# Kernel tuning notes

Measured on AMD Instinct MI355X. Metric: run time of the kernel, lower is better.

Reference implementation:

```python
import jax, jax.numpy as jnp
import numpy as np

BINS = 10
LOSS_WEIGHT = 1.0


def setup_inputs() -> dict:
    key = jax.random.key(0)
    k1, k2 = jax.random.split(key)
    B, C = 16384, 1000
    logits = jax.random.normal(k1, (B, C), dtype=jnp.float32)
    target_indices = jax.random.randint(k2, (B,), 0, C)
    return {"logits": logits, "target_indices": target_indices}


def reference(logits, target_indices):
    B, C = logits.shape
    bins = BINS
    target = jax.nn.one_hot(target_indices, C, dtype=logits.dtype)  # [B, C]
    # gradient-norm proxy (detached in the original)
    g = jnp.abs(jax.nn.sigmoid(jax.lax.stop_gradient(logits)) - target)  # [B, C], in [0, 1]
    tot = jnp.asarray(B * C, logits.dtype)  # all label_weights are 1 -> tot = B*C
    # edges are i/bins with last edge bumped by 1e-6, so bin = clip(floor(g*bins), 0, bins-1)
    bin_idx = jnp.clip((g * bins).astype(jnp.int32), 0, bins - 1)  # [B, C]
    counts = jax.ops.segment_sum(
        jnp.ones((B * C,), logits.dtype), bin_idx.reshape(-1), num_segments=bins
    )  # [bins]
    nonempty = counts > 0
    n = jnp.sum(nonempty).astype(logits.dtype)  # number of non-empty bins
    per_bin_w = jnp.where(nonempty, tot / jnp.maximum(counts, 1.0), 0.0)  # [bins]
    weights = per_bin_w[bin_idx] / jnp.maximum(n, 1.0)  # [B, C]
    weights = jax.lax.stop_gradient(weights)
    # binary_cross_entropy_with_logits, elementwise, stable form
    bce = jnp.maximum(logits, 0.0) - logits * target + jnp.log1p(jnp.exp(-jnp.abs(logits)))
    loss = jnp.sum(weights * bce) / tot
    return loss * LOSS_WEIGHT
```

## Files before the change

### kernel.cpp

```cpp
#include <hip/hip_runtime.h>

typedef float v2f __attribute__((ext_vector_type(2)));

namespace {
constexpr int kB = 16384;
constexpr int kC = 1000;
constexpr int kNElem = kB * kC;
constexpr int kNV4 = kNElem / 4;
constexpr int kV4PerRow = kC / 4;
constexpr int kBlocks = 1280;
constexpr int kThreads = 256;
constexpr int kS = kBlocks * kThreads;
}


__device__ __forceinline__ void ghmc_elem(float L, float& bce, unsigned& bin)
{
    const float kLn2   = 0.6931471805599453f;
    const float kNRLn2 = -1.4426950408889634f;
    const float en  = __builtin_amdgcn_exp2f(kNRLn2 * fabsf(L));
    const float den = 1.f + en;
    const float lg  = __builtin_amdgcn_logf(den);
    const float r   = __builtin_amdgcn_rcpf(den);
    bce = fmaf(lg, kLn2, fmaxf(L, 0.f));
    unsigned babs = (unsigned)(10.f * r);
    babs = babs > 9u ? 9u : babs;
    bin = (L >= 0.f) ? babs : 9u - babs;
}

__device__ __forceinline__ void proc4(const float4 v, int dt,
    v2f& a01, v2f& a23, v2f& a45, v2f& a67, v2f& a89,
    unsigned long long& hcnt,
    const v2f C01, const v2f C23, const v2f C45, const v2f C67, const v2f C89)
{
    const float lv[4] = {v.x, v.y, v.z, v.w};
    #pragma unroll
    for (int e = 0; e < 4; ++e) {
        float bce; unsigned bin;
        ghmc_elem(lv[e], bce, bin);
        hcnt += 1ull << (6u * bin);
        const v2f b2 = {bce, bce};
        a01 += __builtin_elementwise_max(b2, C01);
        a23 += __builtin_elementwise_max(b2, C23);
        a45 += __builtin_elementwise_max(b2, C45);
        a67 += __builtin_elementwise_max(b2, C67);
        a89 += __builtin_elementwise_max(b2, C89);
    }
    if (__builtin_expect((unsigned)dt < 4u, 0)) {
        float L = v.x;
        L = (dt == 1) ? v.y : L;
        L = (dt == 2) ? v.z : L;
        L = (dt == 3) ? v.w : L;
        float bn_; unsigned bnb;
        ghmc_elem(L, bn_, bnb);
        const float bt_ = bn_ - L;
        const unsigned babs = (bnb >= 5u) ? bnb : 9u - bnb;
        const unsigned btb  = (L <= 0.f) ? babs : 9u - babs;
        hcnt += (1ull << (6u * btb)) - (1ull << (6u * bnb));
        const v2f bn2 = {bn_, bn_}, bt2 = {bt_, bt_};
        a01 += __builtin_elementwise_max(bt2, C01) - __builtin_elementwise_max(bn2, C01);
        a23 += __builtin_elementwise_max(bt2, C23) - __builtin_elementwise_max(bn2, C23);
        a45 += __builtin_elementwise_max(bt2, C45) - __builtin_elementwise_max(bn2, C45);
        a67 += __builtin_elementwise_max(bt2, C67) - __builtin_elementwise_max(bn2, C67);
        a89 += __builtin_elementwise_max(bt2, C89) - __builtin_elementwise_max(bn2, C89);
    }
}

__device__ __forceinline__ int dt_for(const int* __restrict__ tgt, int i)
{
    const int row = i / kV4PerRow;
    return tgt[row] - (i - row * kV4PerRow) * 4;
}

__global__ __launch_bounds__(kThreads) void ghmc_main(
    const float* __restrict__ logits,
    const int* __restrict__ tgt,
    float* __restrict__ pf,
    unsigned* __restrict__ pu)
{
    const v2f C01 = {0.0f,        0.10536052f};
    const v2f C23 = {0.22314355f, 0.35667494f};
    const v2f C45 = {0.51082562f, 0.69314718f};
    const v2f C67 = {0.91629073f, 1.20397280f};
    const v2f C89 = {1.60943791f, 2.30258509f};

    v2f a01 = {0.f,0.f}, a23 = {0.f,0.f}, a45 = {0.f,0.f},
        a67 = {0.f,0.f}, a89 = {0.f,0.f};
    unsigned long long hcnt = 0ull;

    const int gid = blockIdx.x * blockDim.x + threadIdx.x;
    const int n = (kNV4 - 1 - gid) / kS + 1;
    const float4* __restrict__ Lp = reinterpret_cast<const float4*>(logits);

    auto ld = [&](int idx) {
        idx = idx < kNV4 ? idx : kNV4 - 1;
        return Lp[idx];
    };

    int i = gid;
    float4 q0 = ld(i), q1 = ld(i + kS), q2 = ld(i + 2 * kS);

    int k = 0;
    for (; k + 4 <= n; k += 4) {
        float4 q3 = ld(i + 3 * kS);
        proc4(q0, dt_for(tgt, i),          a01, a23, a45, a67, a89, hcnt, C01, C23, C45, C67, C89);
        q0 = ld(i + 4 * kS);
        proc4(q1, dt_for(tgt, i + kS),     a01, a23, a45, a67, a89, hcnt, C01, C23, C45, C67, C89);
        q1 = ld(i + 5 * kS);
        proc4(q2, dt_for(tgt, i + 2 * kS), a01, a23, a45, a67, a89, hcnt, C01, C23, C45, C67, C89);
        q2 = ld(i + 6 * kS);
        proc4(q3, dt_for(tgt, i + 3 * kS), a01, a23, a45, a67, a89, hcnt, C01, C23, C45, C67, C89);
        i += 4 * kS;
    }
    for (; k < n; ++k) {
        proc4(q0, dt_for(tgt, i), a01, a23, a45, a67, a89, hcnt, C01, C23, C45, C67, C89);
        q0 = q1; q1 = q2;
        i += kS;
    }

    unsigned long long lo = 0ull, hi = 0ull;
    #pragma unroll
    for (int j = 0; j < 5; ++j) {
        lo += ((hcnt >> (6 * j))       & 63ull) << (12 * j);
        hi += ((hcnt >> (6 * (j + 5))) & 63ull) << (12 * j);
    }
    float r10[10] = {a01.x, a01.y, a23.x, a23.y, a45.x, a45.y, a67.x, a67.y, a89.x, a89.y};
    #pragma unroll
    for (int off = 32; off > 0; off >>= 1) {
        #pragma unroll
        for (int j = 0; j < 10; ++j) r10[j] += __shfl_down(r10[j], off);
        lo += __shfl_down(lo, off);
        hi += __shfl_down(hi, off);
    }

    __shared__ float              sf[4][10];
    __shared__ unsigned long long sc[4][2];
    const int wave = threadIdx.x >> 6;
    const int lane = threadIdx.x & 63;
    if (lane == 0) {
        #pragma unroll
        for (int j = 0; j < 10; ++j) sf[wave][j] = r10[j];
        sc[wave][0] = lo; sc[wave][1] = hi;
    }
    __syncthreads();
    const int t = threadIdx.x;
    if (t < 10) {
        pf[t * kBlocks + blockIdx.x] = sf[0][t] + sf[1][t] + sf[2][t] + sf[3][t];
    } else if (t < 20) {
        const int b = t - 10;
        const int half = (b < 5) ? 0 : 1;
        const int sh = 12 * (b < 5 ? b : b - 5);
        unsigned s = 0;
        #pragma unroll
        for (int w = 0; w < 4; ++w) s += (unsigned)((sc[w][half] >> sh) & 4095ull);
        pu[b * kBlocks + blockIdx.x] = s;
    }
}

__global__ __launch_bounds__(640) void ghmc_reduce(
    const float* __restrict__ pf,
    const unsigned* __restrict__ pu,
    float* __restrict__ out)
{
    const int wave = threadIdx.x >> 6;
    const int lane = threadIdx.x & 63;

    const float4* pf4 = reinterpret_cast<const float4*>(pf + wave * kBlocks);
    const uint4*  pu4 = reinterpret_cast<const uint4*>(pu + wave * kBlocks);
    double   fs = 0.0;
    unsigned cs = 0u;
    #pragma unroll
    for (int it = 0; it < kBlocks / 256; ++it) {
        const float4 f = pf4[lane + it * 64];
        const uint4  u = pu4[lane + it * 64];
        fs += (double)f.x + (double)f.y + (double)f.z + (double)f.w;
        cs += u.x + u.y + u.z + u.w;
    }
    #pragma unroll
    for (int off = 32; off > 0; off >>= 1) {
        fs += __shfl_down(fs, off);
        cs += __shfl_down(cs, off);
    }

    __shared__ double   sF[10];
    __shared__ unsigned sC[10];
    if (lane == 0) { sF[wave] = fs; sC[wave] = cs; }
    __syncthreads();

    if (threadIdx.x == 0) {
        const double cj[10] = {0.0,
            0.10536051565782630, 0.22314355131420976, 0.35667494393873245,
            0.51082562376599072, 0.69314718055994531, 0.91629073187415511,
            1.20397280432593600, 1.60943791243410040, 2.30258509299404570};
        double N[10], cnt[11], cum[11];
        for (int j = 0; j < 10; ++j) N[j] = (double)sC[j];
        cnt[10] = 0.0;
        for (int j = 9; j >= 0; --j) cnt[j] = cnt[j + 1] + N[j];
        cum[10] = 0.0;
        cum[0] = sF[0];
        for (int j = 1; j <= 9; ++j)
            cum[j] = sF[j] - cj[j] * ((double)kNElem - cnt[j]);
        double loss = 0.0, n = 0.0;
        for (int j = 0; j < 10; ++j) {
            if (N[j] > 0.0) { n += 1.0; loss += (cum[j] - cum[j + 1]) / N[j]; }
        }
        out[0] = (float)(loss / (n > 1.0 ? n : 1.0));
    }
}

extern "C" void kernel_launch(void* const* d_in, const int* in_sizes, int n_in,
                              void* d_out, int out_size, void* d_ws, size_t ws_size,
                              hipStream_t stream)
{
    const float* logits = (const float*)d_in[0];
    const int*   tgt    = (const int*)d_in[1];
    float*    pf = (float*)d_ws;
    unsigned* pu = (unsigned*)((char*)d_ws + 10 * kBlocks * 4);
    ghmc_main<<<kBlocks, kThreads, 0, stream>>>(logits, tgt, pf, pu);
    ghmc_reduce<<<1, 640, 0, stream>>>(pf, pu, (float*)d_out);
}
```

Before: 31.87 us.

## Size grid for exact per-thread trip count and fully unroll main loop

Raises the block count so each thread processes exactly eight float4 vectors, removing bounds clamping and the remainder loop. All target-offset lookups are hoisted ahead of processing, and four loads are kept in flight in a fully unrolled loop. The reduction kernel switches to scalar strided loads because the new block count is not a multiple of 256. This adds register pressure and more blocks in exchange for less loop and index overhead.

```diff
diff --git a/kernel.cpp b/kernel.cpp
--- a/kernel.cpp
+++ b/kernel.cpp
@@ -8,9 +8,10 @@
 constexpr int kNElem = kB * kC;
 constexpr int kNV4 = kNElem / 4;
 constexpr int kV4PerRow = kC / 4;
-constexpr int kBlocks = 1280;
+constexpr int kBlocks = 2000;
 constexpr int kThreads = 256;
 constexpr int kS = kBlocks * kThreads;
+constexpr int kN = 8;
 }
 
 
@@ -66,12 +67,6 @@
     }
 }
 
-__device__ __forceinline__ int dt_for(const int* __restrict__ tgt, int i)
-{
-    const int row = i / kV4PerRow;
-    return tgt[row] - (i - row * kV4PerRow) * 4;
-}
-
 __global__ __launch_bounds__(kThreads) void ghmc_main(
     const float* __restrict__ logits,
     const int* __restrict__ tgt,
@@ -88,34 +83,24 @@
         a67 = {0.f,0.f}, a89 = {0.f,0.f};
     unsigned long long hcnt = 0ull;
 
-    const int gid = blockIdx.x * blockDim.x + threadIdx.x;
-    const int n = (kNV4 - 1 - gid) / kS + 1;
+    const int gid = blockIdx.x * kThreads + threadIdx.x;
     const float4* __restrict__ Lp = reinterpret_cast<const float4*>(logits);
 
-    auto ld = [&](int idx) {
-        idx = idx < kNV4 ? idx : kNV4 - 1;
-        return Lp[idx];
-    };
-
-    int i = gid;
-    float4 q0 = ld(i), q1 = ld(i + kS), q2 = ld(i + 2 * kS);
-
-    int k = 0;
-    for (; k + 4 <= n; k += 4) {
-        float4 q3 = ld(i + 3 * kS);
-        proc4(q0, dt_for(tgt, i),          a01, a23, a45, a67, a89, hcnt, C01, C23, C45, C67, C89);
-        q0 = ld(i + 4 * kS);
-        proc4(q1, dt_for(tgt, i + kS),     a01, a23, a45, a67, a89, hcnt, C01, C23, C45, C67, C89);
-        q1 = ld(i + 5 * kS);
-        proc4(q2, dt_for(tgt, i + 2 * kS), a01, a23, a45, a67, a89, hcnt, C01, C23, C45, C67, C89);
-        q2 = ld(i + 6 * kS);
-        proc4(q3, dt_for(tgt, i + 3 * kS), a01, a23, a45, a67, a89, hcnt, C01, C23, C45, C67, C89);
-        i += 4 * kS;
-    }
-    for (; k < n; ++k) {
-        proc4(q0, dt_for(tgt, i), a01, a23, a45, a67, a89, hcnt, C01, C23, C45, C67, C89);
-        q0 = q1; q1 = q2;
-        i += kS;
+    float4 q[kN];
+    int    dt[kN];
+
+    #pragma unroll
+    for (int k = 0; k < 4; ++k) q[k] = Lp[gid + k * kS];
+    #pragma unroll
+    for (int k = 0; k < kN; ++k) {
+        const int i = gid + k * kS;
+        const int row = i / kV4PerRow;
+        dt[k] = tgt[row] - (i - row * kV4PerRow) * 4;
+    }
+    #pragma unroll
+    for (int k = 0; k < kN; ++k) {
+        if (k < 4) q[k + 4] = Lp[gid + (k + 4) * kS];
+        proc4(q[k], dt[k], a01, a23, a45, a67, a89, hcnt, C01, C23, C45, C67, C89);
     }
 
     unsigned long long lo = 0ull, hi = 0ull;
@@ -165,16 +150,12 @@
     const int wave = threadIdx.x >> 6;
     const int lane = threadIdx.x & 63;
 
-    const float4* pf4 = reinterpret_cast<const float4*>(pf + wave * kBlocks);
-    const uint4*  pu4 = reinterpret_cast<const uint4*>(pu + wave * kBlocks);
     double   fs = 0.0;
     unsigned cs = 0u;
-    #pragma unroll
-    for (int it = 0; it < kBlocks / 256; ++it) {
-        const float4 f = pf4[lane + it * 64];
-        const uint4  u = pu4[lane + it * 64];
-        fs += (double)f.x + (double)f.y + (double)f.z + (double)f.w;
-        cs += u.x + u.y + u.z + u.w;
+    #pragma unroll 8
+    for (int b = lane; b < kBlocks; b += 64) {
+        fs += (double)pf[wave * kBlocks + b];
+        cs += pu[wave * kBlocks + b];
     }
     #pragma unroll
     for (int off = 32; off > 0; off >>= 1) {
```

Measured after the change: 34.04 us. 6.8% more time.
